# Kernel optimization log

Measured on AMD Instinct MI355X. Metric: run time of the kernel, lower is better.

The kernel has to match this reference:

```python
import jax, jax.numpy as jnp
import numpy as np

N = 50000      # nodes
E = 800000     # edges
D = 128        # d_model
H = 8          # heads
DH = D // H    # head dim
FF = 512       # dim_ff
NB = 32        # degree buckets
EPS = 1e-5


def _ln(x, g, b):
    mu = jnp.mean(x, axis=-1, keepdims=True)
    var = jnp.mean((x - mu) ** 2, axis=-1, keepdims=True)
    return (x - mu) * jax.lax.rsqrt(var + EPS) * g + b


def setup_inputs() -> dict:
    key = jax.random.key(0)
    ks = jax.random.split(key, 12)
    s = 0.02
    return {
        'x': jax.random.normal(ks[0], (N, D), jnp.float32),
        'row': jnp.sort(jax.random.randint(ks[1], (E,), 0, N, jnp.int32)),
        'col': jax.random.randint(ks[2], (E,), 0, N, jnp.int32),
        'deg_bucket': jax.random.randint(ks[3], (N,), 0, NB, jnp.int32),
        'Wq': jax.random.normal(ks[4], (D, D), jnp.float32) * s,
        'bq': jnp.zeros((D,), jnp.float32),
        'Wk': jax.random.normal(ks[5], (D, D), jnp.float32) * s,
        'bk': jnp.zeros((D,), jnp.float32),
        'Wv': jax.random.normal(ks[6], (D, D), jnp.float32) * s,
        'bv': jnp.zeros((D,), jnp.float32),
        'Wo': jax.random.normal(ks[7], (D, D), jnp.float32) * s,
        'bo': jnp.zeros((D,), jnp.float32),
        'emb': jax.random.normal(ks[8], (NB, H), jnp.float32) * s,
        'ln1_g': jnp.ones((D,), jnp.float32), 'ln1_b': jnp.zeros((D,), jnp.float32),
        'ln2_g': jnp.ones((D,), jnp.float32), 'ln2_b': jnp.zeros((D,), jnp.float32),
        'W1': jax.random.normal(ks[9], (D, FF), jnp.float32) * s,
        'b1': jnp.zeros((FF,), jnp.float32),
        'W2': jax.random.normal(ks[10], (FF, D), jnp.float32) * s,
        'b2': jnp.zeros((D,), jnp.float32),
    }


def reference(x, row, col, deg_bucket, Wq, bq, Wk, bk, Wv, bv, Wo, bo, emb,
              ln1_g, ln1_b, ln2_g, ln2_b, W1, b1, W2, b2):
    scale = DH ** (-0.5)
    Q = (x @ Wq + bq).reshape(N, H, DH)
    K = (x @ Wk + bk).reshape(N, H, DH)
    V = (x @ Wv + bv).reshape(N, H, DH)
    # edge-wise QK dot products: [E, H]
    scores = jnp.einsum('ehd,ehd->eh', Q[row], K[col]) * scale
    scores = scores + emb[deg_bucket[row]] + emb[deg_bucket[col]]
    # segment softmax over destination node `row`
    max_s = jax.ops.segment_max(scores, row, num_segments=N, indices_are_sorted=True)
    exp_s = jnp.exp(scores - max_s[row])
    sum_s = jax.ops.segment_sum(exp_s, row, num_segments=N, indices_are_sorted=True)
    alpha = exp_s / jnp.maximum(sum_s[row], 1e-12)
    # scatter-weighted aggregation of V[col]: [N, H, DH]
    agg = jax.ops.segment_sum(alpha[..., None] * V[col], row, num_segments=N,
                              indices_are_sorted=True)
    out = agg.reshape(N, D) @ Wo + bo
    h = _ln(x + out, ln1_g, ln1_b)
    ffo = jax.nn.gelu(h @ W1 + b1, approximate=False) @ W2 + b2
    return _ln(h + ffo, ln2_g, ln2_b)
```

## Files before the change

### kernel.cpp

```cpp
#include <hip/hip_runtime.h>
#include <math.h>

#define NN 50000
#define NE 800000
#define DM 128
#define NH 8
#define FF 512
#define NBLK 391
#define NBLK64 782

#define PB_X    6250
#define PB_WT   192
#define PB_RP   196
#define PB_EMB  1563
#define PB_TOT  (PB_X + PB_WT + PB_RP + PB_EMB)

typedef __attribute__((ext_vector_type(8))) short bf16x8;
typedef __attribute__((ext_vector_type(4))) float f32x4;
typedef __attribute__((ext_vector_type(2))) float f32x2;

__device__ __forceinline__ short f2bf(float f) {
    union { float f; unsigned u; } v; v.f = f;
    unsigned r = v.u + 0x7fff + ((v.u >> 16) & 1);
    return (short)(r >> 16);
}
__device__ __forceinline__ float bf2f(short s) {
    union { unsigned u; float f; } v; v.u = ((unsigned)(unsigned short)s) << 16;
    return v.f;
}
__device__ __forceinline__ unsigned char f2fp8(float f) {
    int p = __builtin_amdgcn_cvt_pk_fp8_f32(f, f, 0, false);
    return (unsigned char)(p & 0xff);
}

__device__ __forceinline__ float gelu_f(float x) {
    float u = x * (0.7978845608f + 0.0356774081f * x * x);
    float t = 1.f - 2.f / (__expf(2.f * u) + 1.f);
    return 0.5f * x * (1.f + t);
}

__device__ __forceinline__ void gload16(const void* g, void* l) {
    __builtin_amdgcn_global_load_lds(
        (const __attribute__((address_space(1))) void*)g,
        (__attribute__((address_space(3))) void*)l, 16, 0, 0);
}

__device__ __forceinline__ void stage_tile(const short* __restrict__ src, int row0,
                                           int maxrow, int ld, int col0,
                                           short* sm) {
    const int tid = threadIdx.x;
    const int w = tid >> 6, l = tid & 63;
    const int p = l & 15;
    #pragma unroll
    for (int j = 0; j < 8; ++j) {
        int lr = w * 32 + j * 4 + (l >> 4);
        int gr = row0 + lr; gr = gr > maxrow ? maxrow : gr;
        int s = p ^ (lr & 7);
        const short* g = src + (size_t)gr * ld + col0 + s * 8;
        gload16(g, sm + (w * 32 + j * 4) * 128);
    }
}

template <int R>
__device__ __forceinline__ void stage_tile_f8(const unsigned char* __restrict__ src,
                                              int row0, int maxrow, int ld, int col0,
                                              unsigned char* sm) {
    const int tid = threadIdx.x;
    const int w = tid >> 6, l = tid & 63;
    const int p = l & 7;
    const int rsub = l >> 3;
    #pragma unroll
    for (int j = 0; j < (R >> 5); ++j) {
        int lr = w * (R >> 2) + j * 8 + rsub;
        int gr = row0 + lr; gr = gr > maxrow ? maxrow : gr;
        int g = p ^ (lr & 7);
        const unsigned char* gp = src + (size_t)gr * ld + col0 + g * 16;
        gload16(gp, sm + (w * (R >> 2) + j * 8) * 128);
    }
}

__device__ __forceinline__ bf16x8 frag_ld(const short* sm, int outer, int slot) {
    return *(const bf16x8*)(sm + outer * 128 + ((slot ^ (outer & 7)) << 3));
}

__device__ __forceinline__ long frag_ld_f8(const unsigned char* sm, int outer, int slot) {
    return *(const long*)(sm + outer * 128 +
                          (((slot >> 1) ^ (outer & 7)) << 4) + ((slot & 1) << 3));
}

__device__ __forceinline__ void mfma_tile(const short* sA, const short* sB,
                                          int wm, int wn, int lane,
                                          f32x4 acc[4][4]) {
    const int l15 = lane & 15, l4 = lane >> 4;
    #pragma unroll
    for (int ks = 0; ks < 4; ++ks) {
        bf16x8 a[4], b[4];
        int slot = ks * 4 + l4;
        #pragma unroll
        for (int f = 0; f < 4; ++f) a[f] = frag_ld(sA, wm * 64 + f * 16 + l15, slot);
        #pragma unroll
        for (int f = 0; f < 4; ++f) b[f] = frag_ld(sB, wn * 64 + f * 16 + l15, slot);
        #pragma unroll
        for (int fm = 0; fm < 4; ++fm)
            #pragma unroll
            for (int fn = 0; fn < 4; ++fn)
                acc[fm][fn] = __builtin_amdgcn_mfma_f32_16x16x32_bf16(
                    a[fm], b[fn], acc[fm][fn], 0, 0, 0);
    }
}

__device__ __forceinline__ void mfma_tile64_f8(const unsigned char* sA,
                                               const unsigned char* sB,
                                               int wm, int wn, int lane,
                                               f32x4 acc[2][4]) {
    const int l15 = lane & 15, l4 = lane >> 4;
    #pragma unroll
    for (int ks = 0; ks < 4; ++ks) {
        long a[2], b[4];
        int slot = ks * 4 + l4;
        #pragma unroll
        for (int f = 0; f < 2; ++f) a[f] = frag_ld_f8(sA, wm * 32 + f * 16 + l15, slot);
        #pragma unroll
        for (int f = 0; f < 4; ++f) b[f] = frag_ld_f8(sB, wn * 64 + f * 16 + l15, slot);
        #pragma unroll
        for (int fm = 0; fm < 2; ++fm)
            #pragma unroll
            for (int fn = 0; fn < 4; ++fn)
                acc[fm][fn] = __builtin_amdgcn_mfma_f32_16x16x32_fp8_fp8(
                    a[fm], b[fn], acc[fm][fn], 0, 0, 0);
    }
}

__global__ __launch_bounds__(256) void k_prep(
    const float* __restrict__ x, short* __restrict__ xb,
    const float* __restrict__ Wq, const float* __restrict__ Wk,
    const float* __restrict__ Wv, const float* __restrict__ Wo,
    const float* __restrict__ W1, const float* __restrict__ W2,
    short* __restrict__ wts,
    unsigned char* __restrict__ w1f8, unsigned char* __restrict__ w2f8,
    const int* __restrict__ row, int* __restrict__ rowptr,
    const int* __restrict__ db, const float* __restrict__ emb,
    float* __restrict__ embn)
{
    int bid = blockIdx.x;
    const int tid = threadIdx.x;

    if (bid < PB_X) {
        int i = bid * 256 + tid;
        if (i < NN * DM / 4) {
            float4 v = ((const float4*)x)[i];
            ((short4*)xb)[i] = make_short4(f2bf(v.x), f2bf(v.y), f2bf(v.z), f2bf(v.w));
        }
        return;
    }
    bid -= PB_X;
    if (bid < PB_WT) {
        const float* W; int K, N, bx, by;
        short* Wt = nullptr; unsigned char* Wf8 = nullptr;
        if (bid < 64) {
            int wsel = bid >> 4, rel = bid & 15;
            W = wsel == 0 ? Wq : wsel == 1 ? Wk : wsel == 2 ? Wv : Wo;
            Wt = wts + wsel * 16384; K = 128; N = 128; bx = rel & 3; by = rel >> 2;
        } else if (bid < 128) {
            int rel = bid - 64;
            W = W1; Wf8 = w1f8; K = 128; N = 512; bx = rel & 15; by = rel >> 4;
        } else {
            int rel = bid - 128;
            W = W2; Wf8 = w2f8; K = 512; N = 128; bx = rel & 3; by = rel >> 2;
        }
        __shared__ float t[32][33];
        int n0 = bx * 32, k0 = by * 32;
        int r = tid >> 3, c4 = (tid & 7) * 4;
        float4 v = *(const float4*)(W + (size_t)(k0 + r) * N + n0 + c4);
        t[r][c4 + 0] = v.x; t[r][c4 + 1] = v.y; t[r][c4 + 2] = v.z; t[r][c4 + 3] = v.w;
        __syncthreads();
        if (Wt) {
            short4 o = make_short4(f2bf(t[c4 + 0][r]), f2bf(t[c4 + 1][r]),
                                   f2bf(t[c4 + 2][r]), f2bf(t[c4 + 3][r]));
            *(short4*)(Wt + (size_t)(n0 + r) * K + k0 + c4) = o;
        } else {
            uchar4 o = make_uchar4(f2fp8(16.f * t[c4 + 0][r]), f2fp8(16.f * t[c4 + 1][r]),
                                   f2fp8(16.f * t[c4 + 2][r]), f2fp8(16.f * t[c4 + 3][r]));
            *(uchar4*)(Wf8 + (size_t)(n0 + r) * K + k0 + c4) = o;
        }
        return;
    }
    bid -= PB_WT;
    if (bid < PB_RP) {
        int n = bid * 256 + tid;
        if (n > NN) return;
        int lo = 0, hi = NE;
        while (lo < hi) {
            int mid = (lo + hi) >> 1;
            if (row[mid] < n) lo = mid + 1; else hi = mid;
        }
        rowptr[n] = lo;
        return;
    }
    bid -= PB_RP;
    {
        int i = bid * 256 + tid;
        if (i < NN * NH) embn[i] = emb[db[i >> 3] * NH + (i & 7)];
    }
}

__global__ __launch_bounds__(256) void k_gemm_qkv(
    const short* __restrict__ xb, const short* __restrict__ Wt,
    const float* __restrict__ bq, const float* __restrict__ bk,
    const float* __restrict__ bv,
    short* __restrict__ Qb, unsigned char* __restrict__ Kf8,
    unsigned char* __restrict__ Vf8)
{
    __shared__ short sm[2 * 16384];
    const int tid = threadIdx.x, lane = tid & 63, wid = tid >> 6;
    const int wm = wid >> 1, wn = wid & 1;
    const int r0 = blockIdx.x * 128;

    stage_tile(xb, r0, NN - 1, 128, 0, sm);
    #pragma unroll
    for (int m = 0; m < 3; ++m) {
        if (m) __syncthreads();
        stage_tile(Wt + m * 16384, 0, 127, 128, 0, sm + 16384);
        __syncthreads();
        f32x4 acc[4][4];
        #pragma unroll
        for (int i = 0; i < 4; ++i)
            #pragma unroll
            for (int j = 0; j < 4; ++j)
                acc[i][j] = (f32x4){0.f, 0.f, 0.f, 0.f};
        mfma_tile(sm, sm + 16384, wm, wn, lane, acc);

        const float* bias = m == 0 ? bq : (m == 1 ? bk : bv);
        #pragma unroll
        for (int fn = 0; fn < 4; ++fn) {
            int col = wn * 64 + fn * 16 + (lane & 15);
            float bc = bias[col];
            #pragma unroll
            for (int fm = 0; fm < 4; ++fm) {
                int rowb = r0 + wm * 64 + fm * 16 + (lane >> 4) * 4;
                #pragma unroll
                for (int rr = 0; rr < 4; ++rr) {
                    int gr = rowb + rr;
                    if (gr < NN) {
                        float v = acc[fm][fn][rr] + bc;
                        if (m == 0)
                            Qb[(size_t)gr * DM + col] = f2bf(v);
                        else if (m == 1)
                            Kf8[(size_t)gr * DM + col] = f2fp8(v);
                        else
                            Vf8[(size_t)gr * DM + col] = f2fp8(v);
                    }
                }
            }
        }
    }
}

__global__ __launch_bounds__(256) void k_attn_wave(
    const short* __restrict__ Qb, const unsigned char* __restrict__ Kf8,
    const unsigned char* __restrict__ Vf8, const int* __restrict__ col,
    const int* __restrict__ rowptr, const float* __restrict__ embn,
    short* __restrict__ aggb)
{
    const int lane = threadIdx.x & 63;
    const int n = blockIdx.x * 4 + (threadIdx.x >> 6);
    const int e0 = rowptr[n], e1 = rowptr[n + 1];
    const int s = lane >> 3, h = lane & 7;
    const int h2 = lane >> 3;

    float qf[16];
    {
        const bf16x8* qp = (const bf16x8*)(Qb + (size_t)n * DM + h * 16);
        bf16x8 q0 = qp[0], q1 = qp[1];
        #pragma unroll
        for (int j = 0; j < 8; ++j) { qf[j] = bf2f(q0[j]); qf[8 + j] = bf2f(q1[j]); }
    }
    const float embr = embn[(size_t)n * NH + h];

    float m = -INFINITY, l = 0.f, acc0 = 0.f, acc1 = 0.f;

    for (int c0 = e0; c0 < e1; c0 += 16) {
        int ea = c0 + s, eb = c0 + 8 + s;
        bool va = ea < e1, vb = eb < e1;
        int ca = col[va ? ea : e1 - 1];
        int cb = col[vb ? eb : e1 - 1];

        int4 kwa = *(const int4*)(Kf8 + (size_t)ca * DM + h * 16);
        int4 kwb = *(const int4*)(Kf8 + (size_t)cb * DM + h * 16);
        float ema = embn[(size_t)ca * NH + h];
        float emB = embn[(size_t)cb * NH + h];

        int nv = e1 - c0; nv = nv > 16 ? 16 : nv;
        unsigned short vv[16];
        #pragma unroll
        for (int j = 0; j < 8; ++j) {
            int cj = __shfl(ca, j * 8);
            vv[j] = (j < nv) ? *(const unsigned short*)(Vf8 + (size_t)cj * DM + lane * 2) : 0;
        }
        #pragma unroll
        for (int j = 0; j < 8; ++j) {
            int cj = __shfl(cb, j * 8);
            vv[8 + j] = (8 + j < nv) ? *(const unsigned short*)(Vf8 + (size_t)cj * DM + lane * 2) : 0;
        }

        float da = 0.f, dbv = 0.f;
        {
            int ka[4] = {kwa.x, kwa.y, kwa.z, kwa.w};
            int kb[4] = {kwb.x, kwb.y, kwb.z, kwb.w};
            #pragma unroll
            for (int w = 0; w < 4; ++w) {
                f32x2 alo = __builtin_amdgcn_cvt_pk_f32_fp8(ka[w], false);
                f32x2 ahi = __builtin_amdgcn_cvt_pk_f32_fp8(ka[w], true);
                f32x2 blo = __builtin_amdgcn_cvt_pk_f32_fp8(kb[w], false);
                f32x2 bhi = __builtin_amdgcn_cvt_pk_f32_fp8(kb[w], true);
                da  += qf[w * 4 + 0] * alo[0] + qf[w * 4 + 1] * alo[1]
                     + qf[w * 4 + 2] * ahi[0] + qf[w * 4 + 3] * ahi[1];
                dbv += qf[w * 4 + 0] * blo[0] + qf[w * 4 + 1] * blo[1]
                     + qf[w * 4 + 2] * bhi[0] + qf[w * 4 + 3] * bhi[1];
            }
        }
        float sa = va ? da * 0.25f + embr + ema : -INFINITY;
        float sb = vb ? dbv * 0.25f + embr + emB : -INFINITY;

        float mc = fmaxf(sa, sb);
        mc = fmaxf(mc, __shfl_xor(mc, 8));
        mc = fmaxf(mc, __shfl_xor(mc, 16));
        mc = fmaxf(mc, __shfl_xor(mc, 32));
        float mn = fmaxf(m, mc);
        float f = __expf(m - mn);
        m = mn;
        float pa = __expf(sa - mn);
        float pb = __expf(sb - mn);
        float ps = pa + pb;
        ps += __shfl_xor(ps, 8);
        ps += __shfl_xor(ps, 16);
        ps += __shfl_xor(ps, 32);
        l = l * f + ps;

        float fr = __shfl(f, h2);
        acc0 *= fr; acc1 *= fr;
        #pragma unroll
        for (int j = 0; j < 8; ++j) {
            float pj = __shfl(pa, j * 8 + h2);
            f32x2 vd = __builtin_amdgcn_cvt_pk_f32_fp8((int)vv[j], false);
            acc0 += pj * vd[0];
            acc1 += pj * vd[1];
        }
        #pragma unroll
        for (int j = 0; j < 8; ++j) {
            float pj = __shfl(pb, j * 8 + h2);
            f32x2 vd = __builtin_amdgcn_cvt_pk_f32_fp8((int)vv[8 + j], false);
            acc0 += pj * vd[0];
            acc1 += pj * vd[1];
        }
    }
    float la = __shfl(l, h2);
    la = fmaxf(la, 1e-12f);
    unsigned o = ((unsigned)(unsigned short)f2bf(acc0 / la)) |
                 (((unsigned)(unsigned short)f2bf(acc1 / la)) << 16);
    *(unsigned*)(aggb + (size_t)n * DM + lane * 2) = o;
}

__global__ __launch_bounds__(256) void k_gemm_ln1(
    const short* __restrict__ aggb, const short* __restrict__ Wot,
    const float* __restrict__ bo, const float* __restrict__ x,
    const float* __restrict__ g, const float* __restrict__ b,
    float* __restrict__ h, unsigned char* __restrict__ hb8)
{
    __shared__ union { short ab[2 * 16384]; float hs[128 * 129]; } u;
    __shared__ float mu[128], rsd[128];
    const int tid = threadIdx.x, lane = tid & 63, wid = tid >> 6;
    const int wm = wid >> 1, wn = wid & 1;
    const int r0 = blockIdx.x * 128;

    stage_tile(aggb, r0, NN - 1, 128, 0, u.ab);
    stage_tile(Wot, 0, 127, 128, 0, u.ab + 16384);
    __syncthreads();

    f32x4 acc[4][4];
    #pragma unroll
    for (int i = 0; i < 4; ++i)
        #pragma unroll
        for (int j = 0; j < 4; ++j) acc[i][j] = (f32x4){0.f, 0.f, 0.f, 0.f};
    mfma_tile(u.ab, u.ab + 16384, wm, wn, lane, acc);
    __syncthreads();

    #pragma unroll
    for (int fn = 0; fn < 4; ++fn) {
        int col = wn * 64 + fn * 16 + (lane & 15);
        float bc = bo[col];
        #pragma unroll
        for (int fm = 0; fm < 4; ++fm) {
            int rowb = wm * 64 + fm * 16 + (lane >> 4) * 4;
            #pragma unroll
            for (int rr = 0; rr < 4; ++rr) {
                int r_ = rowb + rr, gr = r0 + r_;
                float xr = (gr < NN) ? x[(size_t)gr * DM + col] : 0.f;
                u.hs[r_ * 129 + col] = acc[fm][fn][rr] + bc + xr;
            }
        }
    }
    __syncthreads();

    {
        int rrow = tid >> 1, half = tid & 1;
        float s = 0.f, q = 0.f;
        #pragma unroll 8
        for (int c = 0; c < 64; ++c) {
            float v = u.hs[rrow * 129 + half * 64 + c];
            s += v; q += v * v;
        }
        s += __shfl_xor(s, 1);
        q += __shfl_xor(q, 1);
        float m = s * (1.f / DM);
        float var = q * (1.f / DM) - m * m;
        if (half == 0) { mu[rrow] = m; rsd[rrow] = rsqrtf(var + 1e-5f); }
    }
    __syncthreads();

    for (int i = 0; i < 64; ++i) {
        int idx = i * 256 + tid;
        int rrow = idx >> 7, c = idx & 127;
        int gr = r0 + rrow;
        if (gr < NN) {
            float v = (u.hs[rrow * 129 + c] - mu[rrow]) * rsd[rrow] * g[c] + b[c];
            h[(size_t)gr * DM + c] = v;
            hb8[(size_t)gr * DM + c] = f2fp8(v);
        }
    }
}

__global__ __launch_bounds__(256) void k_ffn_fused(
    const unsigned char* __restrict__ hb8, const unsigned char* __restrict__ W1f8,
    const float* __restrict__ b1, const unsigned char* __restrict__ W2f8,
    const float* __restrict__ b2, const float* __restrict__ h,
    const float* __restrict__ g, const float* __restrict__ bb,
    float* __restrict__ out)
{
    extern __shared__ char smraw[];
    unsigned char* A = (unsigned char*)smraw;
    unsigned char* B = A + 8192;
    unsigned char* C = B + 16384;
    float* hs = (float*)smraw;
    __shared__ float mu[64], rsd[64];

    const int tid = threadIdx.x, lane = tid & 63, wid = tid >> 6;
    const int wm = wid >> 1, wn = wid & 1;
    const int l15 = lane & 15, l4 = lane >> 4;
    const int r0 = blockIdx.x * 64;

    f32x4 acc2[2][4];
    #pragma unroll
    for (int i = 0; i < 2; ++i)
        #pragma unroll
        for (int j = 0; j < 4; ++j) acc2[i][j] = (f32x4){0.f, 0.f, 0.f, 0.f};

    stage_tile_f8<64>(hb8, r0, NN - 1, 128, 0, A);

    for (int kc = 0; kc < 4; ++kc) {
        if (kc) __syncthreads();
        stage_tile_f8<128>(W1f8, kc * 128, FF - 1, 128, 0, B);
        __syncthreads();

        f32x4 accf[2][4];
        #pragma unroll
        for (int i = 0; i < 2; ++i)
            #pragma unroll
            for (int j = 0; j < 4; ++j) accf[i][j] = (f32x4){0.f, 0.f, 0.f, 0.f};
        mfma_tile64_f8(A, B, wm, wn, lane, accf);

        #pragma unroll
        for (int fn = 0; fn < 4; ++fn) {
            int nloc = wn * 64 + fn * 16 + l15;
            float bc = b1[kc * 128 + nloc];
            #pragma unroll
            for (int fm = 0; fm < 2; ++fm) {
                int rowb = wm * 32 + fm * 16 + l4 * 4;
                #pragma unroll
                for (int rr = 0; rr < 4; ++rr) {
                    int row = rowb + rr;
                    float v = 16.f * gelu_f(accf[fm][fn][rr] * 0.0625f + bc);
                    C[row * 128 + ((((nloc >> 4) ^ (row & 7)) << 4) | (nloc & 15))]
                        = f2fp8(v);
                }
            }
        }
        __syncthreads();
        stage_tile_f8<128>(W2f8, 0, 127, 512, kc * 128, B);
        __syncthreads();
        mfma_tile64_f8(C, B, wm, wn, lane, acc2);
    }
    __syncthreads();

    #pragma unroll
    for (int fn = 0; fn < 4; ++fn) {
        int col = wn * 64 + fn * 16 + l15;
        float bc = b2[col];
        #pragma unroll
        for (int fm = 0; fm < 2; ++fm) {
            int rowb = wm * 32 + fm * 16 + l4 * 4;
            #pragma unroll
            for (int rr = 0; rr < 4; ++rr) {
                int r_ = rowb + rr, gr = r0 + r_;
                float hr = (gr < NN) ? h[(size_t)gr * DM + col] : 0.f;
                hs[r_ * 129 + col] = acc2[fm][fn][rr] * (1.f / 256.f) + bc + hr;
            }
        }
    }
    __syncthreads();

    {
        int rrow = tid >> 2, q = tid & 3;
        float s = 0.f, qq = 0.f;
        #pragma unroll 8
        for (int c = 0; c < 32; ++c) {
            float v = hs[rrow * 129 + q * 32 + c];
            s += v; qq += v * v;
        }
        s += __shfl_xor(s, 1);  qq += __shfl_xor(qq, 1);
        s += __shfl_xor(s, 2);  qq += __shfl_xor(qq, 2);
        float m = s * (1.f / DM);
        float var = qq * (1.f / DM) - m * m;
        if (q == 0) { mu[rrow] = m; rsd[rrow] = rsqrtf(var + 1e-5f); }
    }
    __syncthreads();

    for (int i = 0; i < 32; ++i) {
        int idx = i * 256 + tid;
        int rrow = idx >> 7, c = idx & 127;
        int gr = r0 + rrow;
        if (gr < NN)
            out[(size_t)gr * DM + c] =
                (hs[rrow * 129 + c] - mu[rrow]) * rsd[rrow] * g[c] + bb[c];
    }
}

extern "C" void kernel_launch(void* const* d_in, const int* in_sizes, int n_in,
                              void* d_out, int out_size, void* d_ws, size_t ws_size,
                              hipStream_t stream) {
    const float* x   = (const float*)d_in[0];
    const int* row   = (const int*)d_in[1];
    const int* col   = (const int*)d_in[2];
    const int* db    = (const int*)d_in[3];
    const float* Wq  = (const float*)d_in[4];
    const float* bq  = (const float*)d_in[5];
    const float* Wk  = (const float*)d_in[6];
    const float* bk  = (const float*)d_in[7];
    const float* Wv  = (const float*)d_in[8];
    const float* bv  = (const float*)d_in[9];
    const float* Wo  = (const float*)d_in[10];
    const float* bo  = (const float*)d_in[11];
    const float* emb = (const float*)d_in[12];
    const float* g1  = (const float*)d_in[13];
    const float* b1n = (const float*)d_in[14];
    const float* g2  = (const float*)d_in[15];
    const float* b2n = (const float*)d_in[16];
    const float* W1  = (const float*)d_in[17];
    const float* b1  = (const float*)d_in[18];
    const float* W2  = (const float*)d_in[19];
    const float* b2  = (const float*)d_in[20];

    char* W = (char*)d_ws;
    float* embn          = (float*)(W + 0);
    unsigned char* Kf8   = (unsigned char*)(W + 1600000);
    unsigned char* Vf8   = (unsigned char*)(W + 8000000);
    short* aggb   = (short*)(W + 25600000);
    short* xb     = (short*)(W + 38400000);
    short* Qb     = (short*)(W + 51200000);
    float* h      = (float*)(W + 51200000);
    unsigned char* hb8 = (unsigned char*)(W + 76800000);
    short* wts    = (short*)(W + 89600000);
    unsigned char* w1f8 = (unsigned char*)(W + 89731072);
    unsigned char* w2f8 = (unsigned char*)(W + 89796608);
    int* rowptr   = (int*)(W + 89862144);

    k_prep<<<PB_TOT, 256, 0, stream>>>(x, xb, Wq, Wk, Wv, Wo, W1, W2, wts,
                                       w1f8, w2f8, row, rowptr, db, emb, embn);
    k_gemm_qkv<<<NBLK, 256, 0, stream>>>(xb, wts, bq, bk, bv, Qb, Kf8, Vf8);
    k_attn_wave<<<NN / 4, 256, 0, stream>>>(Qb, Kf8, Vf8, col, rowptr, embn, aggb);
    k_gemm_ln1<<<NBLK, 256, 0, stream>>>(aggb, wts + 49152, bo, x, g1, b1n, h, hb8);
    k_ffn_fused<<<NBLK64, 256, 33024, stream>>>(hb8, w1f8, b1, w2f8, b2, h,
                                                g2, b2n, (float*)d_out);
}
```

Measured before the change: 203.9 us.

## Make FFN kernel persistent with W1/W2 resident in LDS and register-level LN2

```diff
diff --git a/kernel.cpp b/kernel.cpp
--- a/kernel.cpp
+++ b/kernel.cpp
@@ -437,101 +437,130 @@
     const float* __restrict__ g, const float* __restrict__ bb,
     float* __restrict__ out)
 {
-    extern __shared__ char smraw[];
-    unsigned char* A = (unsigned char*)smraw;
-    unsigned char* B = A + 8192;
-    unsigned char* C = B + 16384;
-    float* hs = (float*)smraw;
-    __shared__ float mu[64], rsd[64];
+    __shared__ unsigned char W1L[65536];
+    __shared__ unsigned char W2L[65536];
+    __shared__ unsigned char A[8192];
+    __shared__ unsigned char C[8192];
+    __shared__ float2 rowstat[2][64];
 
     const int tid = threadIdx.x, lane = tid & 63, wid = tid >> 6;
     const int wm = wid >> 1, wn = wid & 1;
     const int l15 = lane & 15, l4 = lane >> 4;
-    const int r0 = blockIdx.x * 64;
-
-    f32x4 acc2[2][4];
-    #pragma unroll
-    for (int i = 0; i < 2; ++i)
-        #pragma unroll
-        for (int j = 0; j < 4; ++j) acc2[i][j] = (f32x4){0.f, 0.f, 0.f, 0.f};
-
-    stage_tile_f8<64>(hb8, r0, NN - 1, 128, 0, A);
-
+
+    #pragma unroll
     for (int kc = 0; kc < 4; ++kc) {
-        if (kc) __syncthreads();
-        stage_tile_f8<128>(W1f8, kc * 128, FF - 1, 128, 0, B);
-        __syncthreads();
-
-        f32x4 accf[2][4];
+        stage_tile_f8<128>(W1f8, kc * 128, FF - 1, 128, 0, W1L + kc * 16384);
+        stage_tile_f8<128>(W2f8, 0, 127, 512, kc * 128, W2L + kc * 16384);
+    }
+    int t = blockIdx.x;
+    stage_tile_f8<64>(hb8, t * 64, NN - 1, 128, 0, A);
+    __syncthreads();
+
+    while (true) {
+        const int r0 = t * 64;
+
+        f32x4 acc2[2][4];
         #pragma unroll
         for (int i = 0; i < 2; ++i)
             #pragma unroll
-            for (int j = 0; j < 4; ++j) accf[i][j] = (f32x4){0.f, 0.f, 0.f, 0.f};
-        mfma_tile64_f8(A, B, wm, wn, lane, accf);
-
-        #pragma unroll
-        for (int fn = 0; fn < 4; ++fn) {
-            int nloc = wn * 64 + fn * 16 + l15;
-            float bc = b1[kc * 128 + nloc];
-            #pragma unroll
-            for (int fm = 0; fm < 2; ++fm) {
-                int rowb = wm * 32 + fm * 16 + l4 * 4;
+            for (int j = 0; j < 4; ++j) acc2[i][j] = (f32x4){0.f, 0.f, 0.f, 0.f};
+
+        #pragma unroll
+        for (int kc = 0; kc < 4; ++kc) {
+            f32x4 accf[2][4];
+            #pragma unroll
+            for (int i = 0; i < 2; ++i)
                 #pragma unroll
-                for (int rr = 0; rr < 4; ++rr) {
-                    int row = rowb + rr;
-                    float v = 16.f * gelu_f(accf[fm][fn][rr] * 0.0625f + bc);
-                    C[row * 128 + ((((nloc >> 4) ^ (row & 7)) << 4) | (nloc & 15))]
-                        = f2fp8(v);
+                for (int j = 0; j < 4; ++j) accf[i][j] = (f32x4){0.f, 0.f, 0.f, 0.f};
+            mfma_tile64_f8(A, W1L + kc * 16384, wm, wn, lane, accf);
+
+            if (kc) __syncthreads();
+            #pragma unroll
+            for (int fn = 0; fn < 4; ++fn) {
+                int nloc = wn * 64 + fn * 16 + l15;
+                float bc = b1[kc * 128 + nloc];
+                #pragma unroll
+                for (int fm = 0; fm < 2; ++fm) {
+                    int rowb = wm * 32 + fm * 16 + l4 * 4;
+                    #pragma unroll
+                    for (int rr = 0; rr < 4; ++rr) {
+                        int row = rowb + rr;
+                        float v = 16.f * gelu_f(accf[fm][fn][rr] * 0.0625f + bc);
+                        C[row * 128 + ((((nloc >> 4) ^ (row & 7)) << 4) | (nloc & 15))]
+                            = f2fp8(v);
+                    }
                 }
             }
+            __syncthreads();
+            mfma_tile64_f8(C, W2L + kc * 16384, wm, wn, lane, acc2);
+        }
+
+        const int tn = t + (int)gridDim.x;
+        if (tn < NBLK64)
+            stage_tile_f8<64>(hb8, tn * 64, NN - 1, 128, 0, A);
+
+        float b2c[4];
+        #pragma unroll
+        for (int fn = 0; fn < 4; ++fn) b2c[fn] = b2[wn * 64 + fn * 16 + l15];
+
+        float srow[2][4], qrow[2][4];
+        #pragma unroll
+        for (int fm = 0; fm < 2; ++fm) {
+            #pragma unroll
+            for (int rr = 0; rr < 4; ++rr) {
+                int ml = wm * 32 + fm * 16 + l4 * 4 + rr;
+                int gr = r0 + ml;
+                int cr = gr < NN ? gr : NN - 1;
+                float s = 0.f, ss = 0.f;
+                #pragma unroll
+                for (int fn = 0; fn < 4; ++fn) {
+                    int colc = wn * 64 + fn * 16 + l15;
+                    float hr = h[(size_t)cr * DM + colc];
+                    float v = acc2[fm][fn][rr] * (1.f / 256.f) + b2c[fn] + hr;
+                    acc2[fm][fn][rr] = v;
+                    s += v; ss += v * v;
+                }
+                s += __shfl_xor(s, 1);  ss += __shfl_xor(ss, 1);
+                s += __shfl_xor(s, 2);  ss += __shfl_xor(ss, 2);
+                s += __shfl_xor(s, 4);  ss += __shfl_xor(ss, 4);
+                s += __shfl_xor(s, 8);  ss += __shfl_xor(ss, 8);
+                srow[fm][rr] = s; qrow[fm][rr] = ss;
+            }
+        }
+        if (l15 == 0) {
+            #pragma unroll
+            for (int fm = 0; fm < 2; ++fm)
+                #pragma unroll
+                for (int rr = 0; rr < 4; ++rr)
+                    rowstat[wn][wm * 32 + fm * 16 + l4 * 4 + rr] =
+                        make_float2(srow[fm][rr], qrow[fm][rr]);
         }
         __syncthreads();
-        stage_tile_f8<128>(W2f8, 0, 127, 512, kc * 128, B);
-        __syncthreads();
-        mfma_tile64_f8(C, B, wm, wn, lane, acc2);
-    }
-    __syncthreads();
-
-    #pragma unroll
-    for (int fn = 0; fn < 4; ++fn) {
-        int col = wn * 64 + fn * 16 + l15;
-        float bc = b2[col];
+
         #pragma unroll
         for (int fm = 0; fm < 2; ++fm) {
-            int rowb = wm * 32 + fm * 16 + l4 * 4;
             #pragma unroll
             for (int rr = 0; rr < 4; ++rr) {
-                int r_ = rowb + rr, gr = r0 + r_;
-                float hr = (gr < NN) ? h[(size_t)gr * DM + col] : 0.f;
-                hs[r_ * 129 + col] = acc2[fm][fn][rr] * (1.f / 256.f) + bc + hr;
+                int ml = wm * 32 + fm * 16 + l4 * 4 + rr;
+                int gr = r0 + ml;
+                float2 a0 = rowstat[0][ml], a1 = rowstat[1][ml];
+                float s = a0.x + a1.x, ss = a0.y + a1.y;
+                float mu = s * (1.f / DM);
+                float var = ss * (1.f / DM) - mu * mu;
+                float rs = rsqrtf(var + 1e-5f);
+                if (gr < NN) {
+                    #pragma unroll
+                    for (int fn = 0; fn < 4; ++fn) {
+                        int colc = wn * 64 + fn * 16 + l15;
+                        out[(size_t)gr * DM + colc] =
+                            (acc2[fm][fn][rr] - mu) * rs * g[colc] + bb[colc];
+                    }
+                }
             }
         }
-    }
-    __syncthreads();
-
-    {
-        int rrow = tid >> 2, q = tid & 3;
-        float s = 0.f, qq = 0.f;
-        #pragma unroll 8
-        for (int c = 0; c < 32; ++c) {
-            float v = hs[rrow * 129 + q * 32 + c];
-            s += v; qq += v * v;
-        }
-        s += __shfl_xor(s, 1);  qq += __shfl_xor(qq, 1);
-        s += __shfl_xor(s, 2);  qq += __shfl_xor(qq, 2);
-        float m = s * (1.f / DM);
-        float var = qq * (1.f / DM) - m * m;
-        if (q == 0) { mu[rrow] = m; rsd[rrow] = rsqrtf(var + 1e-5f); }
-    }
-    __syncthreads();
-
-    for (int i = 0; i < 32; ++i) {
-        int idx = i * 256 + tid;
-        int rrow = idx >> 7, c = idx & 127;
-        int gr = r0 + rrow;
-        if (gr < NN)
-            out[(size_t)gr * DM + c] =
-                (hs[rrow * 129 + c] - mu[rrow]) * rsd[rrow] * g[c] + bb[c];
+
+        if (tn >= NBLK64) break;
+        t = tn;
     }
 }
 
@@ -579,6 +608,6 @@
     k_gemm_qkv<<<NBLK, 256, 0, stream>>>(xb, wts, bq, bk, bv, Qb, Kf8, Vf8);
     k_attn_wave<<<NN / 4, 256, 0, stream>>>(Qb, Kf8, Vf8, col, rowptr, embn, aggb);
     k_gemm_ln1<<<NBLK, 256, 0, stream>>>(aggb, wts + 49152, bo, x, g1, b1n, h, hb8);
-    k_ffn_fused<<<NBLK64, 256, 33024, stream>>>(hb8, w1f8, b1, w2f8, b2, h,
-                                                g2, b2n, (float*)d_out);
-}
+    k_ffn_fused<<<256, 256, 0, stream>>>(hb8, w1f8, b1, w2f8, b2, h,
+                                         g2, b2n, (float*)d_out);
+}
```

Measured after the change: 206.8 us. No clear change (+1.4%).
